# Performance work log

Hardware: AMD Instinct MI355X
Metric: run time of the kernel (lower is better)

## Reference

```python
import jax, jax.numpy as jnp
import numpy as np
from jax import lax

BN_EPS = 1e-5

def _tern(w):
    # TWN-style ternarization with straight-through estimator
    d = 0.7 * jnp.mean(jnp.abs(w))
    q = jnp.where(jnp.abs(w) > d, jnp.sign(w), jnp.zeros_like(w))
    return w + lax.stop_gradient(q - w)

def _conv(x, w, b):
    y = lax.conv_general_dilated(x, _tern(w), (1, 1), 'SAME',
                                 dimension_numbers=('NCHW', 'OIHW', 'NCHW'))
    return y + b[None, :, None, None]

def _bn4(x, g, b, m, v):
    inv = g * lax.rsqrt(v + BN_EPS)
    return (x - m[None, :, None, None]) * inv[None, :, None, None] + b[None, :, None, None]

def _bn2(x, g, b, m, v):
    return (x - m) * (g * lax.rsqrt(v + BN_EPS)) + b

def _pool(x):
    return lax.reduce_window(x, -jnp.inf, lax.max, (1, 1, 2, 2), (1, 1, 2, 2), 'VALID')


def setup_inputs() -> dict:
    key = jax.random.key(0)
    ks = jax.random.split(key, 8)
    f = jnp.float32
    d = {}
    d['x'] = jax.random.normal(ks[0], (1024, 1, 28, 28), f)
    wshapes = {'w1': (32, 1, 3, 3), 'w2': (64, 32, 3, 3), 'w3': (128, 64, 3, 3),
               'w4': (128, 128, 3, 3), 'wf1': (256, 6272), 'wf2': (128, 256), 'wf3': (10, 128)}
    for i, (n, s) in enumerate(wshapes.items()):
        d[n] = jax.random.normal(ks[i + 1], s, f) * 0.1
    for n, c in [('1', 32), ('2', 64), ('3', 128), ('4', 128)]:
        d['b' + n] = jnp.zeros((c,), f)
        d['g' + n] = jnp.ones((c,), f)
        d['be' + n] = jnp.zeros((c,), f)
        d['m' + n] = jnp.zeros((c,), f)
        d['v' + n] = jnp.ones((c,), f)
    for n, c in [('f1', 256), ('f2', 128)]:
        d['b' + n] = jnp.zeros((c,), f)
        d['g' + n] = jnp.ones((c,), f)
        d['be' + n] = jnp.zeros((c,), f)
        d['m' + n] = jnp.zeros((c,), f)
        d['v' + n] = jnp.ones((c,), f)
    d['bf3'] = jnp.zeros((10,), f)
    return d


def reference(x, w1, b1, g1, be1, m1, v1, w2, b2, g2, be2, m2, v2,
              w3, b3, g3, be3, m3, v3, w4, b4, g4, be4, m4, v4,
              wf1, bf1, gf1, bef1, mf1, vf1, wf2, bf2, gf2, bef2, mf2, vf2,
              wf3, bf3):
    h = jax.nn.relu(_bn4(_conv(x, w1, b1), g1, be1, m1, v1))
    h = jax.nn.relu(_bn4(_conv(h, w2, b2), g2, be2, m2, v2))
    h = _pool(h)                                  # [B,64,14,14]
    h = jax.nn.relu(_bn4(_conv(h, w3, b3), g3, be3, m3, v3))
    h = jax.nn.relu(_bn4(_conv(h, w4, b4), g4, be4, m4, v4))
    h = _pool(h)                                  # [B,128,7,7]
    h = h.reshape(h.shape[0], -1)                 # [B,6272]
    h = jax.nn.relu(_bn2(h @ _tern(wf1).T + bf1, gf1, bef1, mf1, vf1))
    h = jax.nn.relu(_bn2(h @ _tern(wf2).T + bf2, gf2, bef2, mf2, vf2))
    return h @ _tern(wf3).T + bf3                 # [B,10] logits
```

## Files before the change

kernel.cpp:

```cpp
#include <hip/hip_runtime.h>
#include <hip/hip_bf16.h>

#define BN_EPS 1e-5f

typedef __attribute__((ext_vector_type(8))) short bf16x8;
typedef __attribute__((ext_vector_type(4))) float f32x4;
typedef unsigned short u16;
typedef unsigned int u32;

__device__ __forceinline__ void load16(const void* g, void* l) {
    __builtin_amdgcn_global_load_lds((const __attribute__((address_space(1))) void*)g,
                                     (__attribute__((address_space(3))) void*)l, 16, 0, 0);
}
__device__ __forceinline__ u16 f2b(float v) {
    __hip_bfloat16 h = __float2bfloat16(v);
    return *reinterpret_cast<u16*>(&h);
}
__device__ __forceinline__ float ternq(float x, float d) {
    return (fabsf(x) > d) ? (x > 0.f ? 1.f : -1.f) : 0.f;
}

constexpr size_t ALGN(size_t x) { return (x + 255) & ~(size_t)255; }
constexpr size_t O_SUMS = 0;
constexpr size_t O_W1R  = 256;
constexpr size_t O_WF2Q = ALGN(O_W1R + 288 * 4);
constexpr size_t O_WF3Q = ALGN(O_WF2Q + 32768 * 4);
constexpr size_t O_BQ2  = ALGN(O_WF3Q + 1280 * 4);
constexpr size_t O_BQ3  = ALGN(O_BQ2 + 64 * 288 * 2);
constexpr size_t O_BQ4  = ALGN(O_BQ3 + 128 * 576 * 2);
constexpr size_t O_BQF1 = ALGN(O_BQ4 + 128 * 1152 * 2);
constexpr size_t O_F1   = ALGN(O_BQF1 + (size_t)256 * 6272 * 2);
constexpr size_t O_F2   = ALGN(O_F1 + 1024 * 256 * 4);
constexpr size_t O_ACT1 = ALGN(O_F2 + 1024 * 128 * 4);
constexpr size_t O_ACT2 = ALGN(O_ACT1 + (size_t)1024 * 900 * 32 * 2);
constexpr size_t O_ACT3 = ALGN(O_ACT2 + (size_t)1024 * 256 * 64 * 2);
constexpr size_t O_ACT4 = ALGN(O_ACT3 + (size_t)1024 * 256 * 128 * 2);

__global__ void zero_sums(float* s) { if (threadIdx.x < 8) s[threadIdx.x] = 0.f; }

__device__ void absmean_seg(const float* __restrict__ w, int n4, float* __restrict__ sum,
                            int b0, int nb) {
    __shared__ float sm[256];
    float s = 0.f;
    for (int i = b0 * 256 + threadIdx.x; i < n4; i += nb * 256) {
        float4 v = ((const float4*)w)[i];
        s += fabsf(v.x) + fabsf(v.y) + fabsf(v.z) + fabsf(v.w);
    }
    sm[threadIdx.x] = s;
    __syncthreads();
    for (int o = 128; o > 0; o >>= 1) {
        if (threadIdx.x < o) sm[threadIdx.x] += sm[threadIdx.x + o];
        __syncthreads();
    }
    if (threadIdx.x == 0) atomicAdd(sum, sm[0]);
}

__global__ void absmean_all(const float* w1, const float* w2, const float* w3, const float* w4,
                            const float* wf1, const float* wf2, const float* wf3, float* sums) {
    int b = blockIdx.x;
    if (b < 160)      absmean_seg(wf1, 401408, sums + 4, b, 160);
    else if (b < 192) absmean_seg(w4, 36864, sums + 3, b - 160, 32);
    else if (b < 208) absmean_seg(w3, 18432, sums + 2, b - 192, 16);
    else if (b < 216) absmean_seg(w2, 4608, sums + 1, b - 208, 8);
    else if (b < 224) absmean_seg(wf2, 8192, sums + 5, b - 216, 8);
    else if (b < 225) absmean_seg(w1, 72, sums + 0, 0, 1);
    else              absmean_seg(wf3, 320, sums + 6, 0, 1);
}

__device__ void tern_conv_seg(const float* __restrict__ w, float d, u16* __restrict__ bq,
                              int COUT, int CIN, int b0, int nb) {
    int N = COUT * CIN * 9;
    for (int i = b0 * 256 + threadIdx.x; i < N; i += nb * 256) {
        float q = ternq(w[i], d);
        int co = i / (CIN * 9), r = i % (CIN * 9);
        int ci = r / 9, tap = r % 9;
        bq[(size_t)co * CIN * 9 + tap * CIN + ci] = f2b(q);
    }
}
__device__ void tern_conv_prime_seg(const float* __restrict__ w, float d, u16* __restrict__ bqp,
                                    int CIN, int b0, int nb) {
    int N = 128 * CIN * 9;
    for (int i = b0 * 256 + threadIdx.x; i < N; i += nb * 256) {
        float q = ternq(w[i], d);
        int co = i / (CIN * 9), r = i % (CIN * 9);
        int ci = r / 9, tap = r % 9;
        int k = tap * CIN + ci;
        int s = k >> 5, qd = (k & 31) >> 3, e = k & 7;
        int lane = qd * 16 + (co & 15), nt = co >> 4;
        bqp[((size_t)(s * 8 + nt) * 64 + lane) * 8 + e] = f2b(q);
    }
}
__device__ void tern_f32_seg(const float* __restrict__ w, float d, float* __restrict__ wq,
                             int N, int b0, int nb) {
    for (int i = b0 * 256 + threadIdx.x; i < N; i += nb * 256) wq[i] = ternq(w[i], d);
}

__global__ void tern_all(const float* w1, const float* w2, const float* w3, const float* w4,
                         const float* wf1, const float* wf2, const float* wf3,
                         const float* __restrict__ sums,
                         float* w1r, u16* bq2, u16* bq3p, u16* bq4p, u16* bqf1,
                         float* wf2q, float* wf3q) {
    int b = blockIdx.x;
    if (b < 1) {
        tern_f32_seg(w1, 0.7f * sums[0] / 288.f, w1r, 288, 0, 1);
    } else if (b < 9) {
        tern_conv_seg(w2, 0.7f * sums[1] / 18432.f, bq2, 64, 32, b - 1, 8);
    } else if (b < 41) {
        tern_conv_prime_seg(w3, 0.7f * sums[2] / 73728.f, bq3p, 64, b - 9, 32);
    } else if (b < 105) {
        tern_conv_prime_seg(w4, 0.7f * sums[3] / 147456.f, bq4p, 128, b - 41, 64);
    } else if (b < 617) {
        float d = 0.7f * sums[4] / 1605632.f;
        for (int i = (b - 105) * 256 + threadIdx.x; i < 1605632; i += 512 * 256) {
            float q = ternq(wf1[i], d);
            int j = i / 6272, k = i % 6272;
            int c = k / 49, s = k % 49;
            bqf1[(size_t)j * 6272 + s * 128 + c] = f2b(q);
        }
    } else if (b < 633) {
        tern_f32_seg(wf2, 0.7f * sums[5] / 32768.f, wf2q, 32768, b - 617, 16);
    } else {
        tern_f32_seg(wf3, 0.7f * sums[6] / 1280.f, wf3q, 1280, 0, 1);
    }
}

template<int C, int HP, int HV>
__device__ void border_zero_dev(u16* __restrict__ buf, int i) {
    constexpr int NB = 2 * HP + 2 * HV;
    constexpr int CG = C / 8;
    if (i >= 1024 * NB * CG) return;
    int cg = i % CG, r = i / CG;
    int b = r % NB, n = r / NB;
    int py, px;
    if (b < HP)               { py = 0;                  px = b; }
    else if (b < 2 * HP)      { py = HP - 1;             px = b - HP; }
    else if (b < 2 * HP + HV) { py = b - 2 * HP + 1;     px = 0; }
    else                      { py = b - 2 * HP - HV + 1; px = HP - 1; }
    size_t off = ((size_t)(n * HP + py) * HP + px) * C + cg * 8;
    *(uint4*)(buf + off) = make_uint4(0, 0, 0, 0);
}

__global__ void init_bufs(u16* __restrict__ act1, u16* __restrict__ act2p, float* __restrict__ f1) {
    int b = blockIdx.x, tid = threadIdx.x;
    if (b < 1856) {
        border_zero_dev<32, 30, 28>(act1, b * 256 + tid);
    } else if (b < 3776) {
        border_zero_dev<64, 16, 14>(act2p, (b - 1856) * 256 + tid);
    } else {
        ((float4*)f1)[(b - 3776) * 256 + tid] = make_float4(0.f, 0.f, 0.f, 0.f);
    }
}

__global__ __launch_bounds__(256)
void conv1_direct(const float* __restrict__ x, const float* __restrict__ w1r,
                  const float* __restrict__ bias, const float* __restrict__ gam,
                  const float* __restrict__ bet, const float* __restrict__ mu,
                  const float* __restrict__ var, u16* __restrict__ out) {
    __shared__ float xs[784];
    __shared__ float wsh[288];
    __shared__ float scl[32], sft[32];
    const int n = blockIdx.x, tid = threadIdx.x;
    for (int i = tid; i < 784; i += 256) xs[i] = x[(size_t)n * 784 + i];
    for (int i = tid; i < 288; i += 256) wsh[i] = w1r[i];
    if (tid < 32) {
        float s = gam[tid] * rsqrtf(var[tid] + BN_EPS);
        scl[tid] = s;
        sft[tid] = (bias[tid] - mu[tid]) * s + bet[tid];
    }
    __syncthreads();
    for (int p = tid; p < 784; p += 256) {
        int y = p / 28, xx = p % 28;
        float patch[9];
#pragma unroll
        for (int dy = 0; dy < 3; ++dy)
#pragma unroll
            for (int dx = 0; dx < 3; ++dx) {
                int gy = y + dy - 1, gx = xx + dx - 1;
                patch[dy * 3 + dx] = (gy >= 0 && gy < 28 && gx >= 0 && gx < 28) ? xs[gy * 28 + gx] : 0.f;
            }
        u32 pk[16];
#pragma unroll
        for (int co = 0; co < 32; co += 2) {
            float s0 = 0.f, s1 = 0.f;
#pragma unroll
            for (int t = 0; t < 9; ++t) {
                s0 += wsh[co * 9 + t] * patch[t];
                s1 += wsh[(co + 1) * 9 + t] * patch[t];
            }
            float v0 = fmaxf(s0 * scl[co] + sft[co], 0.f);
            float v1 = fmaxf(s1 * scl[co + 1] + sft[co + 1], 0.f);
            pk[co >> 1] = ((u32)f2b(v1) << 16) | (u32)f2b(v0);
        }
        size_t base = ((size_t)(n * 30 + y + 1) * 30 + (xx + 1)) * 32;
#pragma unroll
        for (int q = 0; q < 4; ++q) ((uint4*)(out + base))[q] = ((uint4*)pk)[q];
    }
}

template<int CIN, int BN, int HV, int HP, int G, bool POOL, bool PADOUT>
__global__ __launch_bounds__(256)
void convgemm(const u16* __restrict__ act, const u16* __restrict__ bq,
              const float* __restrict__ bias, const float* __restrict__ gam,
              const float* __restrict__ bet, const float* __restrict__ mu,
              const float* __restrict__ var, u16* __restrict__ out) {
    constexpr int BM = 128;
    constexpr int K = 9 * CIN;
    constexpr int S = K / (32 * G);
    constexpr int TPC = CIN / 32;
    constexpr int NT = BN / 32;
    constexpr int RB = BN / 64;
    constexpr int HO = HV / 2;
    constexpr int PP = POOL ? HO * HO : HV * HV;

    __shared__ __align__(16) u16 Alds[G][BM * 32];
    __shared__ __align__(16) u16 Blds[G][BN * 32];
    __shared__ int rowA[BM];
    __shared__ int rowO[BM];
    __shared__ float scl[BN], sft[BN];

    const int tid = threadIdx.x;
    const int m0 = blockIdx.x * BM;

    for (int t = tid; t < BM; t += 256) {
        int base;
        if (POOL) {
            int p = (m0 >> 2) + (t >> 2), q = t & 3;
            int n = p / PP, rr = p % PP;
            int oy = rr / HO, ox = rr % HO;
            int y = oy * 2 + (q >> 1), x = ox * 2 + (q & 1);
            base = ((n * HP + y) * HP + x) * CIN;
        } else {
            int m = m0 + t;
            int n = m / PP, rr = m % PP;
            int y = rr / HV, x = rr % HV;
            base = ((n * HP + y) * HP + x) * CIN;
        }
        rowA[t] = base;
    }
    if (POOL) {
        if (tid < 32) {
            int p = (m0 >> 2) + tid;
            int n = p / PP, rr = p % PP;
            int oy = rr / HO, ox = rr % HO;
            rowO[tid] = PADOUT ? ((n * 16 + oy + 1) * 16 + ox + 1) * BN : p * BN;
        }
    } else {
        for (int t = tid; t < BM; t += 256) {
            int m = m0 + t;
            int n = m / PP, rr = m % PP;
            int y = rr / HV, x = rr % HV;
            rowO[t] = PADOUT ? ((n * 16 + y + 1) * 16 + x + 1) * BN : m * BN;
        }
    }
    if (tid < BN) {
        float s = gam[tid] * rsqrtf(var[tid] + BN_EPS);
        scl[tid] = s;
        sft[tid] = (bias[tid] - mu[tid]) * s + bet[tid];
    }
    __syncthreads();

    int arow[2];
    arow[0] = rowA[(tid >> 6) * 16 + (tid & 15)];
    arow[1] = rowA[64 + (tid >> 6) * 16 + (tid & 15)];
    const int chunkb = ((tid >> 4) & 3) * 16;
    const int bco = (tid >> 6) * 16 + (tid & 15);
    const char* actb = (const char*)act;
    const char* bqb  = (const char*)bq;

    const int wave = tid >> 6, lane = tid & 63;
    const int wm = wave & 1, wn = wave >> 1;
    const int fr16 = lane * 16;

    f32x4 acc[4][NT] = {};

    for (int s = 0; s < S; ++s) {
#pragma unroll
        for (int j = 0; j < G; ++j) {
            int g = s * G + j;
            int tap = g / TPC, cio = (g % TPC) * 32;
            int dy = tap / 3, dx = tap % 3;
            int toffb = ((dy * HP + dx) * CIN + cio) * 2;
            char* Al = (char*)Alds[j];
#pragma unroll
            for (int r = 0; r < 2; ++r)
                load16(actb + (size_t)arow[r] * 2 + toffb + chunkb, Al + r * 4096 + tid * 16);
            char* Bl = (char*)Blds[j];
            int bkob = g * 64 + chunkb;
#pragma unroll
            for (int r = 0; r < RB; ++r)
                load16(bqb + (size_t)(r * 64 + bco) * K * 2 + bkob, Bl + r * 4096 + tid * 16);
        }
        __syncthreads();
#pragma unroll
        for (int j = 0; j < G; ++j) {
            const char* Al = (const char*)Alds[j];
            const char* Bl = (const char*)Blds[j];
            bf16x8 af[4], bf[NT];
#pragma unroll
            for (int mt = 0; mt < 4; ++mt)
                af[mt] = *(const bf16x8*)(Al + (wm * 4 + mt) * 1024 + fr16);
#pragma unroll
            for (int nt = 0; nt < NT; ++nt)
                bf[nt] = *(const bf16x8*)(Bl + (wn * NT + nt) * 1024 + fr16);
#pragma unroll
            for (int mt = 0; mt < 4; ++mt)
#pragma unroll
                for (int nt = 0; nt < NT; ++nt)
                    acc[mt][nt] = __builtin_amdgcn_mfma_f32_16x16x32_bf16(af[mt], bf[nt], acc[mt][nt], 0, 0, 0);
        }
        __syncthreads();
    }

    const int fr = lane & 15, quad = lane >> 4;
    if (POOL) {
#pragma unroll
        for (int mt = 0; mt < 4; ++mt) {
            int pl = wm * 16 + mt * 4 + quad;
            int ob = rowO[pl];
#pragma unroll
            for (int nt = 0; nt < NT; ++nt) {
                int col = wn * (NT * 16) + nt * 16 + fr;
                float sc = scl[col], sh = sft[col];
                f32x4 a = acc[mt][nt];
                float v0 = a[0] * sc + sh, v1 = a[1] * sc + sh;
                float v2 = a[2] * sc + sh, v3 = a[3] * sc + sh;
                float mx = fmaxf(fmaxf(v0, v1), fmaxf(v2, v3));
                out[(size_t)ob + col] = f2b(fmaxf(mx, 0.f));
            }
        }
    } else {
#pragma unroll
        for (int mt = 0; mt < 4; ++mt) {
            int rb = wm * 64 + mt * 16 + quad * 4;
            int o0 = rowO[rb], o1 = rowO[rb + 1], o2 = rowO[rb + 2], o3 = rowO[rb + 3];
#pragma unroll
            for (int nt = 0; nt < NT; ++nt) {
                int col = wn * (NT * 16) + nt * 16 + fr;
                float sc = scl[col], sh = sft[col];
                f32x4 a = acc[mt][nt];
                out[(size_t)o0 + col] = f2b(fmaxf(a[0] * sc + sh, 0.f));
                out[(size_t)o1 + col] = f2b(fmaxf(a[1] * sc + sh, 0.f));
                out[(size_t)o2 + col] = f2b(fmaxf(a[2] * sc + sh, 0.f));
                out[(size_t)o3 + col] = f2b(fmaxf(a[3] * sc + sh, 0.f));
            }
        }
    }
}

__global__ __launch_bounds__(256)
void conv34(const u16* __restrict__ act2p, const u16* __restrict__ b3p, const u16* __restrict__ b4p,
            const float* __restrict__ b3, const float* __restrict__ g3, const float* __restrict__ be3,
            const float* __restrict__ m3, const float* __restrict__ v3,
            const float* __restrict__ b4, const float* __restrict__ g4, const float* __restrict__ be4,
            const float* __restrict__ m4, const float* __restrict__ v4,
            u16* __restrict__ out) {
    __shared__ __align__(16) u16 Xs[32768];

    const int tid = threadIdx.x;
    const int n = blockIdx.x;
    const int wave = tid >> 6, lane = tid & 63;
    const int wm = wave & 1, wn = wave >> 1;
    const int fr = lane & 15, quad = lane >> 4;
    char* X = (char*)Xs;

    float scl3[4], sft3[4], scl4[4], sft4[4];
#pragma unroll
    for (int nt = 0; nt < 4; ++nt) {
        int c = wn * 64 + nt * 16 + fr;
        float s = g3[c] * rsqrtf(v3[c] + BN_EPS);
        scl3[nt] = s; sft3[nt] = (b3[c] - m3[c]) * s + be3[c];
        s = g4[c] * rsqrtf(v4[c] + BN_EPS);
        scl4[nt] = s; sft4[nt] = (b4[c] - m4[c]) * s + be4[c];
    }

    {
        const uint4* src = (const uint4*)(act2p + (size_t)n * 16384);
#pragma unroll
        for (int it = 0; it < 8; ++it) {
            int i = it * 256 + tid;
            int r = i >> 3, c = i & 7;
            uint4 v = src[i];
            *(uint4*)(X + r * 128 + ((c ^ (r & 7)) * 16)) = v;
        }
    }
    __syncthreads();

    int r0a[7];
#pragma unroll
    for (int mtl = 0; mtl < 7; ++mtl) {
        int g = wm * 7 + mtl + 1;
        int pxc = min(max(fr, 1), 14);
        r0a[mtl] = (g - 1) * 16 + (pxc - 1);
    }
    f32x4 acc[7][4] = {};
    const char* B3 = (const char*)b3p;
#pragma unroll 3
    for (int s = 0; s < 18; ++s) {
        int tap = s >> 1;
        int rdel = (tap / 3) * 16 + tap % 3;
        int cs = (s & 1) * 4;
        bf16x8 af[7], bf[4];
#pragma unroll
        for (int mtl = 0; mtl < 7; ++mtl) {
            int r = r0a[mtl] + rdel;
            int pos = (cs + quad) ^ (r & 7);
            af[mtl] = *(const bf16x8*)(X + r * 128 + pos * 16);
        }
#pragma unroll
        for (int nt = 0; nt < 4; ++nt)
            bf[nt] = *(const bf16x8*)(B3 + ((size_t)((s * 8 + wn * 4 + nt) * 64 + lane)) * 16);
#pragma unroll
        for (int mtl = 0; mtl < 7; ++mtl)
#pragma unroll
            for (int nt = 0; nt < 4; ++nt)
                acc[mtl][nt] = __builtin_amdgcn_mfma_f32_16x16x32_bf16(af[mtl], bf[nt], acc[mtl][nt], 0, 0, 0);
    }
    __syncthreads();

    for (int t = tid; t < 60 * 16; t += 256) {
        int j = t & 15, b = t >> 4;
        int m = (b < 16) ? b : (b < 32) ? 240 + (b - 16) : (b < 46) ? (b - 31) * 16 : (b - 45) * 16 + 15;
        *(uint4*)(X + m * 256 + j * 16) = make_uint4(0, 0, 0, 0);
    }
#pragma unroll
    for (int mtl = 0; mtl < 7; ++mtl) {
        int g = wm * 7 + mtl + 1;
#pragma unroll
        for (int nt = 0; nt < 4; ++nt) {
            int col = wn * 64 + nt * 16 + fr;
            int c = col >> 3;
            f32x4 a = acc[mtl][nt];
#pragma unroll
            for (int j = 0; j < 4; ++j) {
                int px = quad * 4 + j;
                if (px >= 1 && px <= 14) {
                    int m = g * 16 + px;
                    float v = fmaxf(a[j] * scl3[nt] + sft3[nt], 0.f);
                    *(u16*)(X + m * 256 + ((c ^ (m & 15)) * 16) + (col & 7) * 2) = f2b(v);
                }
            }
        }
    }
    __syncthreads();

    int r0b[7];
#pragma unroll
    for (int mtl = 0; mtl < 7; ++mtl) {
        int m = (wm * 7 + mtl) * 16 + fr;
        int p = min(m >> 2, 48), q = m & 3;
        int y2 = (p / 7) * 2 + (q >> 1), x2 = (p % 7) * 2 + (q & 1);
        r0b[mtl] = y2 * 16 + x2;
    }
    f32x4 acc4[7][4] = {};
    const char* B4 = (const char*)b4p;
#pragma unroll 2
    for (int s = 0; s < 36; ++s) {
        int tap = s >> 2;
        int rdel = (tap / 3) * 16 + tap % 3;
        int cs = (s & 3) * 4;
        bf16x8 af[7], bf[4];
#pragma unroll
        for (int mtl = 0; mtl < 7; ++mtl) {
            int r = r0b[mtl] + rdel;
            int pos = (cs + quad) ^ (r & 15);
            af[mtl] = *(const bf16x8*)(X + r * 256 + pos * 16);
        }
#pragma unroll
        for (int nt = 0; nt < 4; ++nt)
            bf[nt] = *(const bf16x8*)(B4 + ((size_t)((s * 8 + wn * 4 + nt) * 64 + lane)) * 16);
#pragma unroll
        for (int mtl = 0; mtl < 7; ++mtl)
#pragma unroll
            for (int nt = 0; nt < 4; ++nt)
                acc4[mtl][nt] = __builtin_amdgcn_mfma_f32_16x16x32_bf16(af[mtl], bf[nt], acc4[mtl][nt], 0, 0, 0);
    }
#pragma unroll
    for (int mtl = 0; mtl < 7; ++mtl) {
        int p = (wm * 7 + mtl) * 4 + quad;
        if (p < 49) {
#pragma unroll
            for (int nt = 0; nt < 4; ++nt) {
                int col = wn * 64 + nt * 16 + fr;
                f32x4 a = acc4[mtl][nt];
                float v0 = a[0] * scl4[nt] + sft4[nt];
                float v1 = a[1] * scl4[nt] + sft4[nt];
                float v2 = a[2] * scl4[nt] + sft4[nt];
                float v3 = a[3] * scl4[nt] + sft4[nt];
                float mx = fmaxf(fmaxf(v0, v1), fmaxf(v2, v3));
                out[((size_t)n * 49 + p) * 128 + col] = f2b(fmaxf(mx, 0.f));
            }
        }
    }
}

__global__ __launch_bounds__(256)
void fc1gemm(const u16* __restrict__ A, const u16* __restrict__ Bq, float* __restrict__ out) {
    constexpr int K = 6272, KC = 896, S = KC / 64;
    __shared__ __align__(16) u16 Alds[2][128 * 32];
    __shared__ __align__(16) u16 Blds[2][128 * 32];
    const int tid = threadIdx.x;
    const int m0 = blockIdx.x * 128;
    const int n0 = blockIdx.y * 128;
    const int k0 = blockIdx.z * KC;
    const int chunkb = ((tid >> 4) & 3) * 16;
    const int rr = (tid >> 6) * 16 + (tid & 15);
    const char* Ag = (const char*)A;
    const char* Bg = (const char*)Bq;
    const int wave = tid >> 6, lane = tid & 63;
    const int wm = wave & 1, wn = wave >> 1;
    const int fr16 = lane * 16;
    f32x4 acc[4][4] = {};

    for (int s = 0; s < S; ++s) {
#pragma unroll
        for (int j = 0; j < 2; ++j) {
            int kb = (k0 + s * 64 + j * 32) * 2 + chunkb;
            char* Al = (char*)Alds[j];
            char* Bl = (char*)Blds[j];
#pragma unroll
            for (int r = 0; r < 2; ++r) {
                load16(Ag + (size_t)(m0 + r * 64 + rr) * K * 2 + kb, Al + r * 4096 + tid * 16);
                load16(Bg + (size_t)(n0 + r * 64 + rr) * K * 2 + kb, Bl + r * 4096 + tid * 16);
            }
        }
        __syncthreads();
#pragma unroll
        for (int j = 0; j < 2; ++j) {
            const char* Al = (const char*)Alds[j];
            const char* Bl = (const char*)Blds[j];
            bf16x8 af[4], bf[4];
#pragma unroll
            for (int mt = 0; mt < 4; ++mt)
                af[mt] = *(const bf16x8*)(Al + (wm * 4 + mt) * 1024 + fr16);
#pragma unroll
            for (int nt = 0; nt < 4; ++nt)
                bf[nt] = *(const bf16x8*)(Bl + (wn * 4 + nt) * 1024 + fr16);
#pragma unroll
            for (int mt = 0; mt < 4; ++mt)
#pragma unroll
                for (int nt = 0; nt < 4; ++nt)
                    acc[mt][nt] = __builtin_amdgcn_mfma_f32_16x16x32_bf16(af[mt], bf[nt], acc[mt][nt], 0, 0, 0);
        }
        __syncthreads();
    }
    const int fr = lane & 15, quad = lane >> 4;
#pragma unroll
    for (int mt = 0; mt < 4; ++mt) {
        int row = m0 + wm * 64 + mt * 16 + quad * 4;
#pragma unroll
        for (int nt = 0; nt < 4; ++nt) {
            int col = n0 + wn * 64 + nt * 16 + fr;
            f32x4 a = acc[mt][nt];
            atomicAdd(&out[(size_t)(row + 0) * 256 + col], a[0]);
            atomicAdd(&out[(size_t)(row + 1) * 256 + col], a[1]);
            atomicAdd(&out[(size_t)(row + 2) * 256 + col], a[2]);
            atomicAdd(&out[(size_t)(row + 3) * 256 + col], a[3]);
        }
    }
}

__global__ __launch_bounds__(256)
void fc2_kernel(const float* __restrict__ A, const float* __restrict__ Bw,
                const float* __restrict__ bA, const float* __restrict__ gA,
                const float* __restrict__ beA, const float* __restrict__ mA,
                const float* __restrict__ vA,
                const float* __restrict__ bias, const float* __restrict__ gam,
                const float* __restrict__ bet, const float* __restrict__ mu,
                const float* __restrict__ var, float* __restrict__ out) {
    constexpr int Nn = 128, K = 256;
    __shared__ __align__(16) float As[16][68];
    __shared__ __align__(16) float Bs[16][68];
    __shared__ float sclA[256], sftA[256];
    const int tid = threadIdx.x;
    const int n0 = blockIdx.x * 64, m0 = blockIdx.y * 64;
    if (tid < 256) {
        float s = gA[tid] * rsqrtf(vA[tid] + BN_EPS);
        sclA[tid] = s;
        sftA[tid] = (bA[tid] - mA[tid]) * s + beA[tid];
    }
    const int tm = tid >> 4, tn = tid & 15;
    const int lr = tid >> 2, lk = (tid & 3) * 4;
    float acc[4][4] = {};
    __syncthreads();
    for (int k0 = 0; k0 < K; k0 += 16) {
        float4 av = *(const float4*)&A[(size_t)(m0 + lr) * K + k0 + lk];
        float4 bv = *(const float4*)&Bw[(size_t)(n0 + lr) * K + k0 + lk];
        As[lk + 0][lr] = fmaxf(av.x * sclA[k0 + lk + 0] + sftA[k0 + lk + 0], 0.f);
        As[lk + 1][lr] = fmaxf(av.y * sclA[k0 + lk + 1] + sftA[k0 + lk + 1], 0.f);
        As[lk + 2][lr] = fmaxf(av.z * sclA[k0 + lk + 2] + sftA[k0 + lk + 2], 0.f);
        As[lk + 3][lr] = fmaxf(av.w * sclA[k0 + lk + 3] + sftA[k0 + lk + 3], 0.f);
        Bs[lk + 0][lr] = bv.x; Bs[lk + 1][lr] = bv.y; Bs[lk + 2][lr] = bv.z; Bs[lk + 3][lr] = bv.w;
        __syncthreads();
#pragma unroll
        for (int k = 0; k < 16; ++k) {
            float4 a = *(const float4*)&As[k][tm * 4];
            float4 b = *(const float4*)&Bs[k][tn * 4];
            acc[0][0] += a.x * b.x; acc[0][1] += a.x * b.y; acc[0][2] += a.x * b.z; acc[0][3] += a.x * b.w;
            acc[1][0] += a.y * b.x; acc[1][1] += a.y * b.y; acc[1][2] += a.y * b.z; acc[1][3] += a.y * b.w;
            acc[2][0] += a.z * b.x; acc[2][1] += a.z * b.y; acc[2][2] += a.z * b.z; acc[2][3] += a.z * b.w;
            acc[3][0] += a.w * b.x; acc[3][1] += a.w * b.y; acc[3][2] += a.w * b.z; acc[3][3] += a.w * b.w;
        }
        __syncthreads();
    }
#pragma unroll
    for (int i = 0; i < 4; ++i) {
        int row = m0 + tm * 4 + i;
#pragma unroll
        for (int j = 0; j < 4; ++j) {
            int col = n0 + tn * 4 + j;
            float sc = gam[col] * rsqrtf(var[col] + BN_EPS);
            float v = (acc[i][j] + bias[col] - mu[col]) * sc + bet[col];
            out[(size_t)row * Nn + col] = fmaxf(v, 0.f);
        }
    }
}

__global__ __launch_bounds__(256)
void fc3_kernel(const float* __restrict__ A, const float* __restrict__ Bw,
                const float* __restrict__ bias, float* __restrict__ out) {
    int i = blockIdx.x * blockDim.x + threadIdx.x;
    if (i >= 1024 * 10) return;
    int n = i / 10, j = i % 10;
    const float4* a = (const float4*)&A[(size_t)n * 128];
    const float4* b = (const float4*)&Bw[(size_t)j * 128];
    float s = 0.f;
#pragma unroll
    for (int k = 0; k < 32; ++k) {
        float4 x = a[k], y = b[k];
        s += x.x * y.x + x.y * y.y + x.z * y.z + x.w * y.w;
    }
    out[i] = s + bias[j];
}

extern "C" void kernel_launch(void* const* d_in, const int* in_sizes, int n_in,
                              void* d_out, int out_size, void* d_ws, size_t ws_size,
                              hipStream_t stream) {
    (void)in_sizes; (void)n_in; (void)out_size; (void)ws_size;
    const float* x   = (const float*)d_in[0];
    const float* w1  = (const float*)d_in[1];
    const float* w2  = (const float*)d_in[2];
    const float* w3  = (const float*)d_in[3];
    const float* w4  = (const float*)d_in[4];
    const float* wf1 = (const float*)d_in[5];
    const float* wf2 = (const float*)d_in[6];
    const float* wf3 = (const float*)d_in[7];
    auto P = [&](int i) { return (const float*)d_in[i]; };
    char* wsb = (char*)d_ws;
    float* sums = (float*)(wsb + O_SUMS);
    float* w1r  = (float*)(wsb + O_W1R);
    float* wf2q = (float*)(wsb + O_WF2Q);
    float* wf3q = (float*)(wsb + O_WF3Q);
    u16* bq2   = (u16*)(wsb + O_BQ2);
    u16* bq3p  = (u16*)(wsb + O_BQ3);
    u16* bq4p  = (u16*)(wsb + O_BQ4);
    u16* bqf1  = (u16*)(wsb + O_BQF1);
    float* f1  = (float*)(wsb + O_F1);
    float* f2  = (float*)(wsb + O_F2);
    u16* act1  = (u16*)(wsb + O_ACT1);
    u16* act2p = (u16*)(wsb + O_ACT2);
    u16* act4p = (u16*)(wsb + O_ACT4);

    zero_sums<<<1, 64, 0, stream>>>(sums);
    absmean_all<<<226, 256, 0, stream>>>(w1, w2, w3, w4, wf1, wf2, wf3, sums);
    tern_all<<<634, 256, 0, stream>>>(w1, w2, w3, w4, wf1, wf2, wf3, sums,
                                      w1r, bq2, bq3p, bq4p, bqf1, wf2q, wf3q);

    init_bufs<<<4032, 256, 0, stream>>>(act1, act2p, f1);

    conv1_direct<<<1024, 256, 0, stream>>>(x, w1r, P(8), P(9), P(10), P(11), P(12), act1);
    convgemm<32, 64, 28, 30, 1, true, true><<<6272, 256, 0, stream>>>(
        act1, bq2, P(13), P(14), P(15), P(16), P(17), act2p);
    conv34<<<1024, 256, 0, stream>>>(
        act2p, bq3p, bq4p,
        P(18), P(19), P(20), P(21), P(22),
        P(23), P(24), P(25), P(26), P(27), act4p);
    fc1gemm<<<dim3(8, 2, 7), 256, 0, stream>>>(act4p, bqf1, f1);
    fc2_kernel<<<dim3(2, 16), 256, 0, stream>>>(
        f1, wf2q, P(28), P(29), P(30), P(31), P(32),
        P(33), P(34), P(35), P(36), P(37), f2);
    fc3_kernel<<<40, 256, 0, stream>>>(f2, wf3q, P(38), (float*)d_out);
}
```

Measured before the change: 409.4 us.

## Fuse conv1 and conv2+pool into one per-image kernel with LDS-resident activations

Conv1 output is kept in a padded LDS tile per image, and the conv2 implicit GEMM with fused BN, ReLU and 2x2 max-pool runs in the same kernel using MFMA. The w2 weights are repacked into a lane-ready fragment layout so B fragments load straight from global memory. This removes the act1 global round trip, its border-zeroing work, and one kernel launch. In exchange it uses about 68KB of LDS per block, which limits occupancy, and some MFMA tiles are computed and discarded by the padded pass structure.

```diff
diff --git a/kernel.cpp b/kernel.cpp
--- a/kernel.cpp
+++ b/kernel.cpp
@@ -67,14 +67,17 @@
     else              absmean_seg(wf3, 320, sums + 6, 0, 1);
 }
 
-__device__ void tern_conv_seg(const float* __restrict__ w, float d, u16* __restrict__ bq,
-                              int COUT, int CIN, int b0, int nb) {
-    int N = COUT * CIN * 9;
+__device__ void tern_conv_prime64(const float* __restrict__ w, float d, u16* __restrict__ bqp,
+                                  int b0, int nb) {
+    const int N = 64 * 32 * 9;
     for (int i = b0 * 256 + threadIdx.x; i < N; i += nb * 256) {
         float q = ternq(w[i], d);
-        int co = i / (CIN * 9), r = i % (CIN * 9);
+        int co = i / 288, r = i % 288;
         int ci = r / 9, tap = r % 9;
-        bq[(size_t)co * CIN * 9 + tap * CIN + ci] = f2b(q);
+        int k = tap * 32 + ci;
+        int s = k >> 5, qd = (k & 31) >> 3, e = k & 7;
+        int lane = qd * 16 + (co & 15), nt = co >> 4;
+        bqp[((size_t)(s * 4 + nt) * 64 + lane) * 8 + e] = f2b(q);
     }
 }
 __device__ void tern_conv_prime_seg(const float* __restrict__ w, float d, u16* __restrict__ bqp,
@@ -98,13 +101,13 @@
 __global__ void tern_all(const float* w1, const float* w2, const float* w3, const float* w4,
                          const float* wf1, const float* wf2, const float* wf3,
                          const float* __restrict__ sums,
-                         float* w1r, u16* bq2, u16* bq3p, u16* bq4p, u16* bqf1,
+                         float* w1r, u16* bq2p, u16* bq3p, u16* bq4p, u16* bqf1,
                          float* wf2q, float* wf3q) {
     int b = blockIdx.x;
     if (b < 1) {
         tern_f32_seg(w1, 0.7f * sums[0] / 288.f, w1r, 288, 0, 1);
     } else if (b < 9) {
-        tern_conv_seg(w2, 0.7f * sums[1] / 18432.f, bq2, 64, 32, b - 1, 8);
+        tern_conv_prime64(w2, 0.7f * sums[1] / 18432.f, bq2p, b - 1, 8);
     } else if (b < 41) {
         tern_conv_prime_seg(w3, 0.7f * sums[2] / 73728.f, bq3p, 64, b - 9, 32);
     } else if (b < 105) {
@@ -140,34 +143,59 @@
     *(uint4*)(buf + off) = make_uint4(0, 0, 0, 0);
 }
 
-__global__ void init_bufs(u16* __restrict__ act1, u16* __restrict__ act2p, float* __restrict__ f1) {
+__global__ void init_bufs(u16* __restrict__ act2p, float* __restrict__ f1) {
     int b = blockIdx.x, tid = threadIdx.x;
-    if (b < 1856) {
-        border_zero_dev<32, 30, 28>(act1, b * 256 + tid);
-    } else if (b < 3776) {
-        border_zero_dev<64, 16, 14>(act2p, (b - 1856) * 256 + tid);
+    if (b < 1920) {
+        border_zero_dev<64, 16, 14>(act2p, b * 256 + tid);
     } else {
-        ((float4*)f1)[(b - 3776) * 256 + tid] = make_float4(0.f, 0.f, 0.f, 0.f);
+        ((float4*)f1)[(b - 1920) * 256 + tid] = make_float4(0.f, 0.f, 0.f, 0.f);
     }
 }
 
 __global__ __launch_bounds__(256)
-void conv1_direct(const float* __restrict__ x, const float* __restrict__ w1r,
-                  const float* __restrict__ bias, const float* __restrict__ gam,
-                  const float* __restrict__ bet, const float* __restrict__ mu,
-                  const float* __restrict__ var, u16* __restrict__ out) {
+void conv12(const float* __restrict__ x, const float* __restrict__ w1r,
+            const float* __restrict__ b1, const float* __restrict__ g1, const float* __restrict__ be1,
+            const float* __restrict__ m1, const float* __restrict__ v1,
+            const u16* __restrict__ b2p,
+            const float* __restrict__ b2, const float* __restrict__ g2, const float* __restrict__ be2,
+            const float* __restrict__ m2, const float* __restrict__ v2,
+            u16* __restrict__ out) {
+    __shared__ __align__(16) char X1[900 * 72];
     __shared__ float xs[784];
-    __shared__ float wsh[288];
-    __shared__ float scl[32], sft[32];
-    const int n = blockIdx.x, tid = threadIdx.x;
+    __shared__ float w1sh[288];
+    __shared__ float scl1[32], sft1[32];
+
+    const int tid = threadIdx.x;
+    const int n = blockIdx.x;
+    const int wave = tid >> 6, lane = tid & 63;
+    const int fr = lane & 15, quad = lane >> 4;
+
+    float scl2[4], sft2[4];
+#pragma unroll
+    for (int nt = 0; nt < 4; ++nt) {
+        int c = nt * 16 + fr;
+        float s = g2[c] * rsqrtf(v2[c] + BN_EPS);
+        scl2[nt] = s;
+        sft2[nt] = (b2[c] - m2[c]) * s + be2[c];
+    }
+
     for (int i = tid; i < 784; i += 256) xs[i] = x[(size_t)n * 784 + i];
-    for (int i = tid; i < 288; i += 256) wsh[i] = w1r[i];
+    for (int i = tid; i < 288; i += 256) w1sh[i] = w1r[i];
     if (tid < 32) {
-        float s = gam[tid] * rsqrtf(var[tid] + BN_EPS);
-        scl[tid] = s;
-        sft[tid] = (bias[tid] - mu[tid]) * s + bet[tid];
+        float s = g1[tid] * rsqrtf(v1[tid] + BN_EPS);
+        scl1[tid] = s;
+        sft1[tid] = (b1[tid] - m1[tid]) * s + be1[tid];
+    }
+    for (int t = tid; t < 116 * 4; t += 256) {
+        int rr = t >> 2, c = t & 3;
+        int row = (rr < 30) ? rr
+                : (rr < 60) ? 870 + (rr - 30)
+                : (rr < 88) ? (rr - 59) * 30
+                : (rr - 87) * 30 + 29;
+        *(uint4*)(X1 + row * 72 + c * 16) = make_uint4(0, 0, 0, 0);
     }
     __syncthreads();
+
     for (int p = tid; p < 784; p += 256) {
         int y = p / 28, xx = p % 28;
         float patch[9];
@@ -184,164 +212,69 @@
             float s0 = 0.f, s1 = 0.f;
 #pragma unroll
             for (int t = 0; t < 9; ++t) {
-                s0 += wsh[co * 9 + t] * patch[t];
-                s1 += wsh[(co + 1) * 9 + t] * patch[t];
+                s0 += w1sh[co * 9 + t] * patch[t];
+                s1 += w1sh[(co + 1) * 9 + t] * patch[t];
             }
-            float v0 = fmaxf(s0 * scl[co] + sft[co], 0.f);
-            float v1 = fmaxf(s1 * scl[co + 1] + sft[co + 1], 0.f);
-            pk[co >> 1] = ((u32)f2b(v1) << 16) | (u32)f2b(v0);
-        }
-        size_t base = ((size_t)(n * 30 + y + 1) * 30 + (xx + 1)) * 32;
-#pragma unroll
-        for (int q = 0; q < 4; ++q) ((uint4*)(out + base))[q] = ((uint4*)pk)[q];
-    }
-}
-
-template<int CIN, int BN, int HV, int HP, int G, bool POOL, bool PADOUT>
-__global__ __launch_bounds__(256)
-void convgemm(const u16* __restrict__ act, const u16* __restrict__ bq,
-              const float* __restrict__ bias, const float* __restrict__ gam,
-              const float* __restrict__ bet, const float* __restrict__ mu,
-              const float* __restrict__ var, u16* __restrict__ out) {
-    constexpr int BM = 128;
-    constexpr int K = 9 * CIN;
-    constexpr int S = K / (32 * G);
-    constexpr int TPC = CIN / 32;
-    constexpr int NT = BN / 32;
-    constexpr int RB = BN / 64;
-    constexpr int HO = HV / 2;
-    constexpr int PP = POOL ? HO * HO : HV * HV;
-
-    __shared__ __align__(16) u16 Alds[G][BM * 32];
-    __shared__ __align__(16) u16 Blds[G][BN * 32];
-    __shared__ int rowA[BM];
-    __shared__ int rowO[BM];
-    __shared__ float scl[BN], sft[BN];
-
-    const int tid = threadIdx.x;
-    const int m0 = blockIdx.x * BM;
-
-    for (int t = tid; t < BM; t += 256) {
-        int base;
-        if (POOL) {
-            int p = (m0 >> 2) + (t >> 2), q = t & 3;
-            int n = p / PP, rr = p % PP;
-            int oy = rr / HO, ox = rr % HO;
-            int y = oy * 2 + (q >> 1), x = ox * 2 + (q & 1);
-            base = ((n * HP + y) * HP + x) * CIN;
-        } else {
-            int m = m0 + t;
-            int n = m / PP, rr = m % PP;
-            int y = rr / HV, x = rr % HV;
-            base = ((n * HP + y) * HP + x) * CIN;
-        }
-        rowA[t] = base;
-    }
-    if (POOL) {
-        if (tid < 32) {
-            int p = (m0 >> 2) + tid;
-            int n = p / PP, rr = p % PP;
-            int oy = rr / HO, ox = rr % HO;
-            rowO[tid] = PADOUT ? ((n * 16 + oy + 1) * 16 + ox + 1) * BN : p * BN;
-        }
-    } else {
-        for (int t = tid; t < BM; t += 256) {
-            int m = m0 + t;
-            int n = m / PP, rr = m % PP;
-            int y = rr / HV, x = rr % HV;
-            rowO[t] = PADOUT ? ((n * 16 + y + 1) * 16 + x + 1) * BN : m * BN;
-        }
-    }
-    if (tid < BN) {
-        float s = gam[tid] * rsqrtf(var[tid] + BN_EPS);
-        scl[tid] = s;
-        sft[tid] = (bias[tid] - mu[tid]) * s + bet[tid];
+            float v0 = fmaxf(s0 * scl1[co] + sft1[co], 0.f);
+            float v1f = fmaxf(s1 * scl1[co + 1] + sft1[co + 1], 0.f);
+            pk[co >> 1] = ((u32)f2b(v1f) << 16) | (u32)f2b(v0);
+        }
+        char* row = X1 + ((y + 1) * 30 + xx + 1) * 72;
+#pragma unroll
+        for (int q = 0; q < 4; ++q) *(uint4*)(row + q * 16) = ((uint4*)pk)[q];
     }
     __syncthreads();
 
-    int arow[2];
-    arow[0] = rowA[(tid >> 6) * 16 + (tid & 15)];
-    arow[1] = rowA[64 + (tid >> 6) * 16 + (tid & 15)];
-    const int chunkb = ((tid >> 4) & 3) * 16;
-    const int bco = (tid >> 6) * 16 + (tid & 15);
-    const char* actb = (const char*)act;
-    const char* bqb  = (const char*)bq;
-
-    const int wave = tid >> 6, lane = tid & 63;
-    const int wm = wave & 1, wn = wave >> 1;
-    const int fr16 = lane * 16;
-
-    f32x4 acc[4][NT] = {};
-
-    for (int s = 0; s < S; ++s) {
-#pragma unroll
-        for (int j = 0; j < G; ++j) {
-            int g = s * G + j;
-            int tap = g / TPC, cio = (g % TPC) * 32;
-            int dy = tap / 3, dx = tap % 3;
-            int toffb = ((dy * HP + dx) * CIN + cio) * 2;
-            char* Al = (char*)Alds[j];
-#pragma unroll
-            for (int r = 0; r < 2; ++r)
-                load16(actb + (size_t)arow[r] * 2 + toffb + chunkb, Al + r * 4096 + tid * 16);
-            char* Bl = (char*)Blds[j];
-            int bkob = g * 64 + chunkb;
-#pragma unroll
-            for (int r = 0; r < RB; ++r)
-                load16(bqb + (size_t)(r * 64 + bco) * K * 2 + bkob, Bl + r * 4096 + tid * 16);
-        }
-        __syncthreads();
-#pragma unroll
-        for (int j = 0; j < G; ++j) {
-            const char* Al = (const char*)Alds[j];
-            const char* Bl = (const char*)Blds[j];
-            bf16x8 af[4], bf[NT];
-#pragma unroll
-            for (int mt = 0; mt < 4; ++mt)
-                af[mt] = *(const bf16x8*)(Al + (wm * 4 + mt) * 1024 + fr16);
-#pragma unroll
-            for (int nt = 0; nt < NT; ++nt)
-                bf[nt] = *(const bf16x8*)(Bl + (wn * NT + nt) * 1024 + fr16);
-#pragma unroll
-            for (int mt = 0; mt < 4; ++mt)
-#pragma unroll
-                for (int nt = 0; nt < NT; ++nt)
-                    acc[mt][nt] = __builtin_amdgcn_mfma_f32_16x16x32_bf16(af[mt], bf[nt], acc[mt][nt], 0, 0, 0);
-        }
-        __syncthreads();
-    }
-
-    const int fr = lane & 15, quad = lane >> 4;
-    if (POOL) {
-#pragma unroll
-        for (int mt = 0; mt < 4; ++mt) {
-            int pl = wm * 16 + mt * 4 + quad;
-            int ob = rowO[pl];
-#pragma unroll
-            for (int nt = 0; nt < NT; ++nt) {
-                int col = wn * (NT * 16) + nt * 16 + fr;
-                float sc = scl[col], sh = sft[col];
-                f32x4 a = acc[mt][nt];
-                float v0 = a[0] * sc + sh, v1 = a[1] * sc + sh;
-                float v2 = a[2] * sc + sh, v3 = a[3] * sc + sh;
-                float mx = fmaxf(fmaxf(v0, v1), fmaxf(v2, v3));
-                out[(size_t)ob + col] = f2b(fmaxf(mx, 0.f));
-            }
-        }
-    } else {
-#pragma unroll
-        for (int mt = 0; mt < 4; ++mt) {
-            int rb = wm * 64 + mt * 16 + quad * 4;
-            int o0 = rowO[rb], o1 = rowO[rb + 1], o2 = rowO[rb + 2], o3 = rowO[rb + 3];
-#pragma unroll
-            for (int nt = 0; nt < NT; ++nt) {
-                int col = wn * (NT * 16) + nt * 16 + fr;
-                float sc = scl[col], sh = sft[col];
-                f32x4 a = acc[mt][nt];
-                out[(size_t)o0 + col] = f2b(fmaxf(a[0] * sc + sh, 0.f));
-                out[(size_t)o1 + col] = f2b(fmaxf(a[1] * sc + sh, 0.f));
-                out[(size_t)o2 + col] = f2b(fmaxf(a[2] * sc + sh, 0.f));
-                out[(size_t)o3 + col] = f2b(fmaxf(a[3] * sc + sh, 0.f));
+    const char* B2 = (const char*)b2p;
+#pragma unroll 1
+    for (int pass = 0; pass < 3; ++pass) {
+        f32x4 acc[5][4] = {};
+        int r0[5], pp[5];
+        bool val[5];
+#pragma unroll
+        for (int t = 0; t < 5; ++t) {
+            int ti = pass * 5 + t;
+            int tc = wave * 13 + ti;
+            val[t] = (ti < 13) && (tc < 49);
+            int tcc = min(tc, 48);
+            int p = tcc * 4 + (fr >> 2), q = fr & 3;
+            int oy = p / 14, ox = p % 14;
+            int y = 2 * oy + (q >> 1), x2 = 2 * ox + (q & 1);
+            r0[t] = ((y + 1) * 30 + x2 + 1) * 72 + quad * 16;
+            pp[t] = tcc * 4 + quad;
+        }
+#pragma unroll 1
+        for (int s = 0; s < 9; ++s) {
+            int off = ((s / 3 - 1) * 30 + (s % 3 - 1)) * 72;
+            bf16x8 af[5], bf[4];
+#pragma unroll
+            for (int t = 0; t < 5; ++t)
+                af[t] = *(const bf16x8*)(X1 + r0[t] + off);
+#pragma unroll
+            for (int nt = 0; nt < 4; ++nt)
+                bf[nt] = *(const bf16x8*)(B2 + (size_t)((s * 4 + nt) * 64 + lane) * 16);
+#pragma unroll
+            for (int t = 0; t < 5; ++t)
+#pragma unroll
+                for (int nt = 0; nt < 4; ++nt)
+                    acc[t][nt] = __builtin_amdgcn_mfma_f32_16x16x32_bf16(af[t], bf[nt], acc[t][nt], 0, 0, 0);
+        }
+#pragma unroll
+        for (int t = 0; t < 5; ++t) {
+            if (val[t]) {
+                int p = pp[t];
+                int oy = p / 14, ox = p % 14;
+                size_t base = ((size_t)(n * 16 + oy + 1) * 16 + ox + 1) * 64;
+#pragma unroll
+                for (int nt = 0; nt < 4; ++nt) {
+                    f32x4 a = acc[t][nt];
+                    float v0 = a[0] * scl2[nt] + sft2[nt];
+                    float v1f = a[1] * scl2[nt] + sft2[nt];
+                    float v2f = a[2] * scl2[nt] + sft2[nt];
+                    float v3 = a[3] * scl2[nt] + sft2[nt];
+                    float mx = fmaxf(fmaxf(v0, v1f), fmaxf(v2f, v3));
+                    out[base + nt * 16 + fr] = f2b(fmaxf(mx, 0.f));
+                }
             }
         }
     }
@@ -650,26 +583,25 @@
     float* w1r  = (float*)(wsb + O_W1R);
     float* wf2q = (float*)(wsb + O_WF2Q);
     float* wf3q = (float*)(wsb + O_WF3Q);
-    u16* bq2   = (u16*)(wsb + O_BQ2);
+    u16* bq2p  = (u16*)(wsb + O_BQ2);
     u16* bq3p  = (u16*)(wsb + O_BQ3);
     u16* bq4p  = (u16*)(wsb + O_BQ4);
     u16* bqf1  = (u16*)(wsb + O_BQF1);
     float* f1  = (float*)(wsb + O_F1);
     float* f2  = (float*)(wsb + O_F2);
-    u16* act1  = (u16*)(wsb + O_ACT1);
     u16* act2p = (u16*)(wsb + O_ACT2);
     u16* act4p = (u16*)(wsb + O_ACT4);
 
     zero_sums<<<1, 64, 0, stream>>>(sums);
     absmean_all<<<226, 256, 0, stream>>>(w1, w2, w3, w4, wf1, wf2, wf3, sums);
     tern_all<<<634, 256, 0, stream>>>(w1, w2, w3, w4, wf1, wf2, wf3, sums,
-                                      w1r, bq2, bq3p, bq4p, bqf1, wf2q, wf3q);
-
-    init_bufs<<<4032, 256, 0, stream>>>(act1, act2p, f1);
-
-    conv1_direct<<<1024, 256, 0, stream>>>(x, w1r, P(8), P(9), P(10), P(11), P(12), act1);
-    convgemm<32, 64, 28, 30, 1, true, true><<<6272, 256, 0, stream>>>(
-        act1, bq2, P(13), P(14), P(15), P(16), P(17), act2p);
+                                      w1r, bq2p, bq3p, bq4p, bqf1, wf2q, wf3q);
+
+    init_bufs<<<2176, 256, 0, stream>>>(act2p, f1);
+
+    conv12<<<1024, 256, 0, stream>>>(
+        x, w1r, P(8), P(9), P(10), P(11), P(12),
+        bq2p, P(13), P(14), P(15), P(16), P(17), act2p);
     conv34<<<1024, 256, 0, stream>>>(
         act2p, bq3p, bq4p,
         P(18), P(19), P(20), P(21), P(22),
```

New measurement: 428.8 us. 1.05x slower.
